# Kernel tuning notes

Measured on AMD Instinct MI355X. Metric: run time of the kernel, lower is better.

The kernel has to match this reference:

```python
import jax, jax.numpy as jnp
import numpy as np

NUM_CLASSES = 100000   # vocab (input_dim of the layer)
DIM = 256              # embedding dim (output_dim of the layer)
BATCH = 256
NUM_TRUE = 1024        # hardcoded num_true in call()
NUM_SAMPLED = 16384    # hardcoded num_sampled in call()
LOG_RANGE = float(np.log(NUM_CLASSES + 1.0))


def _sample_log_uniform_unique(rng, n, range_max):
    # Mimics tf log_uniform_candidate_sampler with unique=True: rejection-sample
    # from P(c) ~ log((c+2)/(c+1)) until n unique ids are collected.
    seen = {}
    log_range = np.log(range_max + 1.0)
    while len(seen) < n:
        u = rng.uniform(0.0, log_range, size=2 * n)
        ids = np.minimum(np.floor(np.exp(u) - 1.0).astype(np.int64), range_max - 1)
        for v in ids.tolist():
            if len(seen) >= n:
                break
            seen[v] = None
    return np.fromiter(seen.keys(), dtype=np.int64, count=n)


def setup_inputs() -> dict:
    key = jax.random.key(0)
    k1, k2, k3, k4 = jax.random.split(key, 4)
    inputs = jax.random.normal(k1, (BATCH, DIM), jnp.float32)
    # Original inits w/b to zeros; use small random values for a non-degenerate baseline.
    w = jax.random.normal(k2, (NUM_CLASSES, DIM), jnp.float32) * 0.02
    b = jax.random.normal(k3, (NUM_CLASSES,), jnp.float32) * 0.02
    labels = jax.random.randint(k4, (BATCH, NUM_TRUE), 0, NUM_CLASSES, dtype=jnp.int32)
    rng = np.random.default_rng(0)
    sampled = jnp.asarray(_sample_log_uniform_unique(rng, NUM_SAMPLED, NUM_CLASSES), jnp.int32)
    return {"inputs": inputs, "w": w, "b": b, "labels": labels, "sampled": sampled}


def _log_uniform_prob(ids):
    idf = ids.astype(jnp.float32)
    return jnp.log((idf + 2.0) / (idf + 1.0)) / LOG_RANGE


def _expected_count(ids):
    # P(id appears among NUM_SAMPLED unique candidates) = 1 - (1-p)^NUM_SAMPLED
    p = _log_uniform_prob(ids)
    return -jnp.expm1(NUM_SAMPLED * jnp.log1p(-p))


def _sigmoid_xent(logits, target):
    # numerically stable sigmoid cross-entropy, target is a scalar label value
    return jnp.maximum(logits, 0.0) - logits * target + jnp.log1p(jnp.exp(-jnp.abs(logits)))


def reference(inputs, w, b, labels, sampled):
    # true logits: per-example dot with each true class row  [B, T]
    true_w = w[labels]                                    # [B, T, D] gather
    true_logits = jnp.einsum('bd,btd->bt', inputs, true_w) + b[labels]
    true_logits = true_logits - jnp.log(_expected_count(labels))
    # sampled logits: shared candidate set  [B, S]
    sampled_logits = inputs @ w[sampled].T + b[sampled]
    sampled_logits = sampled_logits - jnp.log(_expected_count(sampled))
    # NCE targets: 1/num_true for true classes, 0 for sampled; sum over columns
    true_xent = _sigmoid_xent(true_logits, 1.0 / NUM_TRUE)
    sampled_xent = _sigmoid_xent(sampled_logits, 0.0)
    return true_xent.sum(axis=1) + sampled_xent.sum(axis=1)   # [B]
```

## Files before the change

kernel.cpp:

```cpp
#include <hip/hip_runtime.h>
#include <hip/hip_bf16.h>

#define NUM_CLASSES 100000
#define DIM 256
#define BATCH 256
#define NUM_TRUE 1024
#define NUM_SAMPLED 16384
#define LOG_RANGE 11.51293546492023f
#define INV_LOG_RANGE (1.0f / LOG_RANGE)

#define SBLOCKS 512
#define NBUCKET 3125
#define CAP     512
#define COMB_THREADS 100096

typedef __bf16 bf16x8 __attribute__((ext_vector_type(8)));
typedef float  f32x4  __attribute__((ext_vector_type(4)));

static __device__ __forceinline__ unsigned short f2bf(float f) {
    unsigned int u = __float_as_uint(f);
    unsigned int lsb = (u >> 16) & 1u;
    u += 0x7fffu + lsb;
    return (unsigned short)(u >> 16);
}

static __device__ __forceinline__ float neg_log_ec(int id) {
    float idf = (float)id;
    float p = logf((idf + 2.0f) / (idf + 1.0f)) * INV_LOG_RANGE;
    float ec = -expm1f((float)NUM_SAMPLED * log1pf(-p));
    return -logf(ec);
}

static __device__ __forceinline__ float dot4(float4 a, float4 b) {
    return fmaf(a.x, b.x, fmaf(a.y, b.y, fmaf(a.z, b.z, a.w * b.w)));
}

__global__ __launch_bounds__(256) void comb_kernel(const float* __restrict__ bias,
                                                   const float* __restrict__ inputs,
                                                   const int* __restrict__ labels,
                                                   float* __restrict__ comb,
                                                   unsigned short* __restrict__ inbf,
                                                   int* __restrict__ cursor,
                                                   unsigned int* __restrict__ pairs) {
    int c = blockIdx.x * 256 + threadIdx.x;
    if (c < NUM_CLASSES) comb[c] = bias[c] + neg_log_ec(c);
    if (c < BATCH * DIM) inbf[c] = f2bf(inputs[c]);
    for (int g = c; g < BATCH * NUM_TRUE; g += COMB_THREADS) {
        int lbl = labels[g];
        int bk = lbl >> 5;
        int pos = atomicAdd(&cursor[bk], 1);
        if (pos < CAP)
            pairs[(size_t)bk * CAP + pos] = ((unsigned int)(g >> 10) << 17) | (unsigned int)lbl;
    }
}

union SMem {
    struct { unsigned short lw[32][264]; float cs[32]; } s;
    struct { float rows[32][260]; float cmb[32]; } t;
};

__global__ __launch_bounds__(256) void fused_kernel(const float* __restrict__ inputs,
                                                    const float* __restrict__ w,
                                                    const float* __restrict__ comb,
                                                    const int* __restrict__ sampled,
                                                    const unsigned short* __restrict__ inbf,
                                                    const int* __restrict__ cursor,
                                                    const unsigned int* __restrict__ pairs,
                                                    float* __restrict__ ptrue,
                                                    float* __restrict__ partial) {
    __shared__ SMem u;
    __shared__ float bacc[BATCH];

    const int tid = threadIdx.x;

    if (blockIdx.x < SBLOCKS) {
        const int sblk = blockIdx.x;
        const int s0 = sblk * 32;
        bacc[tid] = 0.0f;

        const int inner = tid & 15;
        const int r16   = tid >> 4;
        #pragma unroll
        for (int rb = 0; rb < 2; ++rb) {
            const int r = rb * 16 + r16;
            const int id = sampled[s0 + r];
            const float* src = w + (size_t)id * DIM;
            #pragma unroll
            for (int j = 0; j < 4; ++j) {
                float4 v = *(const float4*)(src + j * 64 + inner * 4);
                ushort4 pk;
                pk.x = f2bf(v.x); pk.y = f2bf(v.y); pk.z = f2bf(v.z); pk.w = f2bf(v.w);
                *(ushort4*)(&u.s.lw[r][j * 64 + inner * 4]) = pk;
            }
        }
        if (tid < 32) u.s.cs[tid] = comb[sampled[s0 + tid]];
        __syncthreads();

        const int lane = tid & 63;
        const int wv   = tid >> 6;
        const int m    = lane & 15;
        const int quad = lane >> 4;
        const int shalf = (wv >> 1) * 16;
        const int bhalf = (wv & 1) * 128;

        bf16x8 af[8];
        #pragma unroll
        for (int kk = 0; kk < 8; ++kk)
            af[kk] = *(const bf16x8*)(&u.s.lw[shalf + m][kk * 32 + quad * 8]);

        #pragma unroll
        for (int t = 0; t < 8; ++t) {
            const int brow = bhalf + t * 16 + m;
            const unsigned short* bp = inbf + brow * DIM;
            bf16x8 bf[8];
            #pragma unroll
            for (int kk = 0; kk < 8; ++kk)
                bf[kk] = *(const bf16x8*)(bp + kk * 32 + quad * 8);
            f32x4 acc = {0, 0, 0, 0};
            #pragma unroll
            for (int kk = 0; kk < 8; ++kk)
                acc = __builtin_amdgcn_mfma_f32_16x16x32_bf16(af[kk], bf[kk], acc, 0, 0, 0);
            float ps = 0.0f;
            #pragma unroll
            for (int r = 0; r < 4; ++r) {
                float c = u.s.cs[shalf + quad * 4 + r];
                float l = acc[r] + c;
                ps += fmaxf(l, 0.0f) + __logf(1.0f + __expf(-fabsf(l)));
            }
            ps += __shfl_xor(ps, 16); ps += __shfl_xor(ps, 32);
            if (quad == 0) atomicAdd(&bacc[bhalf + t * 16 + m], ps);
        }
        __syncthreads();
        partial[tid * SBLOCKS + sblk] = bacc[tid];
    } else {
        const int tb = blockIdx.x - SBLOCKS;
        int n = cursor[tb];
        n = (n < CAP) ? n : CAP;
        bacc[tid] = 0.0f;

        if (n > 0) {
            const float* wb = w + (size_t)tb * (32 * DIM);
            #pragma unroll
            for (int j = 0; j < 8; ++j) {
                const int e = (tid + j * 256) * 4;
                float4 v = *(const float4*)(wb + e);
                *(float4*)&u.t.rows[e >> 8][e & 255] = v;
            }
            if (tid < 32) u.t.cmb[tid] = comb[tb * 32 + tid];
        }
        __syncthreads();

        if (n > 0) {
            const int gidx = tid >> 4;
            const int part = tid & 15;
            const float4* inp4 = (const float4*)inputs;
            const unsigned int* pb = pairs + (size_t)tb * CAP;
            for (int p = gidx; p < n; p += 16) {
                const unsigned int pk = pb[p];
                const int b = pk >> 17;
                const int r = pk & 31;
                float4 i0 = inp4[b * 64 + part];
                float4 i1 = inp4[b * 64 + 16 + part];
                float4 i2 = inp4[b * 64 + 32 + part];
                float4 i3 = inp4[b * 64 + 48 + part];
                float4 w0 = *(const float4*)&u.t.rows[r][part * 4];
                float4 w1 = *(const float4*)&u.t.rows[r][64 + part * 4];
                float4 w2 = *(const float4*)&u.t.rows[r][128 + part * 4];
                float4 w3 = *(const float4*)&u.t.rows[r][192 + part * 4];
                float d = dot4(w0, i0) + dot4(w1, i1) + dot4(w2, i2) + dot4(w3, i3);
                d += __shfl_xor(d, 1); d += __shfl_xor(d, 2);
                d += __shfl_xor(d, 4); d += __shfl_xor(d, 8);
                const float logit = d + u.t.cmb[r];
                const float v = fmaxf(logit, 0.0f) - logit * (1.0f / (float)NUM_TRUE)
                              + __logf(1.0f + __expf(-fabsf(logit)));
                if (part == 0) atomicAdd(&bacc[b], v);
            }
        }
        __syncthreads();
        ptrue[tb * 256 + tid] = bacc[tid];
    }
}

__global__ __launch_bounds__(256) void reduce_kernel(const float* __restrict__ partial,
                                                     const float* __restrict__ ptrue,
                                                     float* __restrict__ out) {
    __shared__ float wsum[4];
    const int b = blockIdx.x;
    const int tid = threadIdx.x;
    float v = partial[b * SBLOCKS + tid] + partial[b * SBLOCKS + 256 + tid];
    #pragma unroll
    for (int i = 0; i < 13; ++i) {
        const int k = tid * 13 + i;
        if (k < NBUCKET) v += ptrue[k * 256 + b];
    }
    v += __shfl_xor(v, 1);  v += __shfl_xor(v, 2);  v += __shfl_xor(v, 4);
    v += __shfl_xor(v, 8);  v += __shfl_xor(v, 16); v += __shfl_xor(v, 32);
    if ((tid & 63) == 0) wsum[tid >> 6] = v;
    __syncthreads();
    if (tid == 0) out[b] = wsum[0] + wsum[1] + wsum[2] + wsum[3];
}

extern "C" void kernel_launch(void* const* d_in, const int* in_sizes, int n_in,
                              void* d_out, int out_size, void* d_ws, size_t ws_size,
                              hipStream_t stream) {
    const float* inputs  = (const float*)d_in[0];
    const float* w       = (const float*)d_in[1];
    const float* bias    = (const float*)d_in[2];
    const int*   labels  = (const int*)d_in[3];
    const int*   sampled = (const int*)d_in[4];
    float* out = (float*)d_out;

    float*          comb    = (float*)d_ws;
    unsigned short* inbf    = (unsigned short*)((char*)d_ws + 409600);
    float*          partial = (float*)((char*)d_ws + 540672);
    float*          ptrue   = (float*)((char*)d_ws + 1064960);
    int*            cursor  = (int*)((char*)d_ws + 4264960);
    unsigned int*   pairs   = (unsigned int*)((char*)d_ws + 4280320);

    hipMemsetAsync(cursor, 0, NBUCKET * sizeof(int), stream);
    comb_kernel<<<(NUM_CLASSES + 255) / 256, 256, 0, stream>>>(bias, inputs, labels,
                                                               comb, inbf, cursor, pairs);
    fused_kernel<<<SBLOCKS + NBUCKET, 256, 0, stream>>>(inputs, w, comb, sampled,
                                                        inbf, cursor, pairs, ptrue, partial);
    reduce_kernel<<<BATCH, 256, 0, stream>>>(partial, ptrue, out);
}
```

Before: 223.0 us.

## Compute true-class logits densely with bf16 MFMA per bucket instead of gathered dots

Each true-label bucket block now converts its 32 weight rows to bf16 and computes the full 32x256 logit tile against all batch rows with MFMA, storing it in shared memory. Each (batch, label) pair then just looks up its logit and applies the cross-entropy, replacing per-pair fp32 dot products that re-read the input rows. The ptrue layout is transposed so the reduce kernel reads it coalesced. This does far more arithmetic per bucket (dense versus sparse) and lowers true-logit precision to bf16, and it now runs even for buckets with no pairs.

After: 282.7 us. 1.27x slower.

```diff
diff --git a/kernel.cpp b/kernel.cpp
--- a/kernel.cpp
+++ b/kernel.cpp
@@ -11,6 +11,7 @@
 
 #define SBLOCKS 512
 #define NBUCKET 3125
+#define NB2     3328
 #define CAP     512
 #define COMB_THREADS 100096
 
@@ -29,10 +30,6 @@
     float p = logf((idf + 2.0f) / (idf + 1.0f)) * INV_LOG_RANGE;
     float ec = -expm1f((float)NUM_SAMPLED * log1pf(-p));
     return -logf(ec);
-}
-
-static __device__ __forceinline__ float dot4(float4 a, float4 b) {
-    return fmaf(a.x, b.x, fmaf(a.y, b.y, fmaf(a.z, b.z, a.w * b.w)));
 }
 
 __global__ __launch_bounds__(256) void comb_kernel(const float* __restrict__ bias,
@@ -55,8 +52,8 @@
 }
 
 union SMem {
-    struct { unsigned short lw[32][264]; float cs[32]; } s;
-    struct { float rows[32][260]; float cmb[32]; } t;
+    unsigned short lw[32][264];
+    float          lgt[32][257];
 };
 
 __global__ __launch_bounds__(256) void fused_kernel(const float* __restrict__ inputs,
@@ -69,17 +66,25 @@
                                                     float* __restrict__ ptrue,
                                                     float* __restrict__ partial) {
     __shared__ SMem u;
+    __shared__ float cs[32];
     __shared__ float bacc[BATCH];
 
-    const int tid = threadIdx.x;
+    const int tid   = threadIdx.x;
+    const int inner = tid & 15;
+    const int r16   = tid >> 4;
+    const int lane  = tid & 63;
+    const int wv    = tid >> 6;
+    const int m     = lane & 15;
+    const int quad  = lane >> 4;
+    const int shalf = (wv >> 1) * 16;
+    const int bhalf = (wv & 1) * 128;
+
+    bacc[tid] = 0.0f;
 
     if (blockIdx.x < SBLOCKS) {
         const int sblk = blockIdx.x;
         const int s0 = sblk * 32;
-        bacc[tid] = 0.0f;
-
-        const int inner = tid & 15;
-        const int r16   = tid >> 4;
+
         #pragma unroll
         for (int rb = 0; rb < 2; ++rb) {
             const int r = rb * 16 + r16;
@@ -90,23 +95,16 @@
                 float4 v = *(const float4*)(src + j * 64 + inner * 4);
                 ushort4 pk;
                 pk.x = f2bf(v.x); pk.y = f2bf(v.y); pk.z = f2bf(v.z); pk.w = f2bf(v.w);
-                *(ushort4*)(&u.s.lw[r][j * 64 + inner * 4]) = pk;
+                *(ushort4*)(&u.lw[r][j * 64 + inner * 4]) = pk;
             }
         }
-        if (tid < 32) u.s.cs[tid] = comb[sampled[s0 + tid]];
-        __syncthreads();
-
-        const int lane = tid & 63;
-        const int wv   = tid >> 6;
-        const int m    = lane & 15;
-        const int quad = lane >> 4;
-        const int shalf = (wv >> 1) * 16;
-        const int bhalf = (wv & 1) * 128;
+        if (tid < 32) cs[tid] = comb[sampled[s0 + tid]];
+        __syncthreads();
 
         bf16x8 af[8];
         #pragma unroll
         for (int kk = 0; kk < 8; ++kk)
-            af[kk] = *(const bf16x8*)(&u.s.lw[shalf + m][kk * 32 + quad * 8]);
+            af[kk] = *(const bf16x8*)(&u.lw[shalf + m][kk * 32 + quad * 8]);
 
         #pragma unroll
         for (int t = 0; t < 8; ++t) {
@@ -123,7 +121,7 @@
             float ps = 0.0f;
             #pragma unroll
             for (int r = 0; r < 4; ++r) {
-                float c = u.s.cs[shalf + quad * 4 + r];
+                float c = cs[shalf + quad * 4 + r];
                 float l = acc[r] + c;
                 ps += fmaxf(l, 0.0f) + __logf(1.0f + __expf(-fabsf(l)));
             }
@@ -134,50 +132,62 @@
         partial[tid * SBLOCKS + sblk] = bacc[tid];
     } else {
         const int tb = blockIdx.x - SBLOCKS;
+        const int s0 = tb * 32;
+
+        const float* wb = w + (size_t)s0 * DIM;
+        #pragma unroll
+        for (int rb = 0; rb < 2; ++rb) {
+            const int r = rb * 16 + r16;
+            const float* src = wb + r * DIM;
+            #pragma unroll
+            for (int j = 0; j < 4; ++j) {
+                float4 v = *(const float4*)(src + j * 64 + inner * 4);
+                ushort4 pk;
+                pk.x = f2bf(v.x); pk.y = f2bf(v.y); pk.z = f2bf(v.z); pk.w = f2bf(v.w);
+                *(ushort4*)(&u.lw[r][j * 64 + inner * 4]) = pk;
+            }
+        }
+        if (tid < 32) cs[tid] = comb[s0 + tid];
+        __syncthreads();
+
+        bf16x8 af[8];
+        #pragma unroll
+        for (int kk = 0; kk < 8; ++kk)
+            af[kk] = *(const bf16x8*)(&u.lw[shalf + m][kk * 32 + quad * 8]);
+        __syncthreads();
+
+        #pragma unroll
+        for (int t = 0; t < 8; ++t) {
+            const int brow = bhalf + t * 16 + m;
+            const unsigned short* bp = inbf + brow * DIM;
+            bf16x8 bf[8];
+            #pragma unroll
+            for (int kk = 0; kk < 8; ++kk)
+                bf[kk] = *(const bf16x8*)(bp + kk * 32 + quad * 8);
+            f32x4 acc = {0, 0, 0, 0};
+            #pragma unroll
+            for (int kk = 0; kk < 8; ++kk)
+                acc = __builtin_amdgcn_mfma_f32_16x16x32_bf16(af[kk], bf[kk], acc, 0, 0, 0);
+            #pragma unroll
+            for (int r = 0; r < 4; ++r)
+                u.lgt[shalf + quad * 4 + r][brow] = acc[r] + cs[shalf + quad * 4 + r];
+        }
+        __syncthreads();
+
         int n = cursor[tb];
         n = (n < CAP) ? n : CAP;
-        bacc[tid] = 0.0f;
-
-        if (n > 0) {
-            const float* wb = w + (size_t)tb * (32 * DIM);
-            #pragma unroll
-            for (int j = 0; j < 8; ++j) {
-                const int e = (tid + j * 256) * 4;
-                float4 v = *(const float4*)(wb + e);
-                *(float4*)&u.t.rows[e >> 8][e & 255] = v;
-            }
-            if (tid < 32) u.t.cmb[tid] = comb[tb * 32 + tid];
-        }
-        __syncthreads();
-
-        if (n > 0) {
-            const int gidx = tid >> 4;
-            const int part = tid & 15;
-            const float4* inp4 = (const float4*)inputs;
-            const unsigned int* pb = pairs + (size_t)tb * CAP;
-            for (int p = gidx; p < n; p += 16) {
-                const unsigned int pk = pb[p];
-                const int b = pk >> 17;
-                const int r = pk & 31;
-                float4 i0 = inp4[b * 64 + part];
-                float4 i1 = inp4[b * 64 + 16 + part];
-                float4 i2 = inp4[b * 64 + 32 + part];
-                float4 i3 = inp4[b * 64 + 48 + part];
-                float4 w0 = *(const float4*)&u.t.rows[r][part * 4];
-                float4 w1 = *(const float4*)&u.t.rows[r][64 + part * 4];
-                float4 w2 = *(const float4*)&u.t.rows[r][128 + part * 4];
-                float4 w3 = *(const float4*)&u.t.rows[r][192 + part * 4];
-                float d = dot4(w0, i0) + dot4(w1, i1) + dot4(w2, i2) + dot4(w3, i3);
-                d += __shfl_xor(d, 1); d += __shfl_xor(d, 2);
-                d += __shfl_xor(d, 4); d += __shfl_xor(d, 8);
-                const float logit = d + u.t.cmb[r];
-                const float v = fmaxf(logit, 0.0f) - logit * (1.0f / (float)NUM_TRUE)
-                              + __logf(1.0f + __expf(-fabsf(logit)));
-                if (part == 0) atomicAdd(&bacc[b], v);
-            }
-        }
-        __syncthreads();
-        ptrue[tb * 256 + tid] = bacc[tid];
+        const unsigned int* pb = pairs + (size_t)tb * CAP;
+        for (int p = tid; p < n; p += 256) {
+            const unsigned int pk = pb[p];
+            const int b = pk >> 17;
+            const int r = pk & 31;
+            const float l = u.lgt[r][b];
+            const float v = fmaxf(l, 0.0f) - l * (1.0f / (float)NUM_TRUE)
+                          + __logf(1.0f + __expf(-fabsf(l)));
+            atomicAdd(&bacc[b], v);
+        }
+        __syncthreads();
+        ptrue[tid * NB2 + tb] = bacc[tid];
     }
 }
 
@@ -190,8 +200,8 @@
     float v = partial[b * SBLOCKS + tid] + partial[b * SBLOCKS + 256 + tid];
     #pragma unroll
     for (int i = 0; i < 13; ++i) {
-        const int k = tid * 13 + i;
-        if (k < NBUCKET) v += ptrue[k * 256 + b];
+        const int k = i * 256 + tid;
+        if (k < NBUCKET) v += ptrue[b * NB2 + k];
     }
     v += __shfl_xor(v, 1);  v += __shfl_xor(v, 2);  v += __shfl_xor(v, 4);
     v += __shfl_xor(v, 8);  v += __shfl_xor(v, 16); v += __shfl_xor(v, 32);
@@ -214,8 +224,8 @@
     unsigned short* inbf    = (unsigned short*)((char*)d_ws + 409600);
     float*          partial = (float*)((char*)d_ws + 540672);
     float*          ptrue   = (float*)((char*)d_ws + 1064960);
-    int*            cursor  = (int*)((char*)d_ws + 4264960);
-    unsigned int*   pairs   = (unsigned int*)((char*)d_ws + 4280320);
+    int*            cursor  = (int*)((char*)d_ws + 4472832);
+    unsigned int*   pairs   = (unsigned int*)((char*)d_ws + 4485632);
 
     hipMemsetAsync(cursor, 0, NBUCKET * sizeof(int), stream);
     comb_kernel<<<(NUM_CLASSES + 255) / 256, 256, 0, stream>>>(bias, inputs, labels,
```

## Compute full dense logits per class bucket with MFMA, mask sampled, reuse for true pairs

Applied to the files above, without the earlier changes.

Replaces the separate sampled-gather GEMM and scalar true-label dot products with a single dense bf16 MFMA pass over all vocabulary rows in 32-class buckets. Each block computes all 256x32 logits into shared memory, sums sigmoid-xent for classes flagged as sampled via a byte mask, and looks up true-pair logits from the same tile. This removes the scattered gather and the fp32 per-pair dot products, but computes logits for every class, about six times the sampled GEMM work, and true logits now use bf16 precision.

Result: slower. 239.0 us (+7.2%).

```diff
diff --git a/kernel.cpp b/kernel.cpp
--- a/kernel.cpp
+++ b/kernel.cpp
@@ -9,7 +9,6 @@
 #define LOG_RANGE 11.51293546492023f
 #define INV_LOG_RANGE (1.0f / LOG_RANGE)
 
-#define SBLOCKS 512
 #define NBUCKET 3125
 #define CAP     512
 #define COMB_THREADS 100096
@@ -31,20 +30,19 @@
     return -logf(ec);
 }
 
-static __device__ __forceinline__ float dot4(float4 a, float4 b) {
-    return fmaf(a.x, b.x, fmaf(a.y, b.y, fmaf(a.z, b.z, a.w * b.w)));
-}
-
 __global__ __launch_bounds__(256) void comb_kernel(const float* __restrict__ bias,
                                                    const float* __restrict__ inputs,
                                                    const int* __restrict__ labels,
+                                                   const int* __restrict__ sampled,
                                                    float* __restrict__ comb,
                                                    unsigned short* __restrict__ inbf,
+                                                   unsigned char* __restrict__ sam,
                                                    int* __restrict__ cursor,
                                                    unsigned int* __restrict__ pairs) {
     int c = blockIdx.x * 256 + threadIdx.x;
     if (c < NUM_CLASSES) comb[c] = bias[c] + neg_log_ec(c);
     if (c < BATCH * DIM) inbf[c] = f2bf(inputs[c]);
+    if (c < NUM_SAMPLED) sam[sampled[c]] = 1;
     for (int g = c; g < BATCH * NUM_TRUE; g += COMB_THREADS) {
         int lbl = labels[g];
         int bk = lbl >> 5;
@@ -54,144 +52,118 @@
     }
 }
 
-union SMem {
-    struct { unsigned short lw[32][264]; float cs[32]; } s;
-    struct { float rows[32][260]; float cmb[32]; } t;
-};
-
-__global__ __launch_bounds__(256) void fused_kernel(const float* __restrict__ inputs,
-                                                    const float* __restrict__ w,
+__global__ __launch_bounds__(256) void fused_kernel(const float* __restrict__ w,
                                                     const float* __restrict__ comb,
-                                                    const int* __restrict__ sampled,
                                                     const unsigned short* __restrict__ inbf,
+                                                    const unsigned char* __restrict__ sam,
                                                     const int* __restrict__ cursor,
                                                     const unsigned int* __restrict__ pairs,
-                                                    float* __restrict__ ptrue,
-                                                    float* __restrict__ partial) {
-    __shared__ SMem u;
+                                                    float* __restrict__ ptrue) {
+    __shared__ unsigned short lw[32][264];
+    __shared__ float lgt[BATCH][33];
+    __shared__ float cs[32];
+    __shared__ int   sf[32];
     __shared__ float bacc[BATCH];
 
     const int tid = threadIdx.x;
+    const int tb  = blockIdx.x;
+    const int s0  = tb * 32;
 
-    if (blockIdx.x < SBLOCKS) {
-        const int sblk = blockIdx.x;
-        const int s0 = sblk * 32;
-        bacc[tid] = 0.0f;
+    int n = cursor[tb];
+    n = (n < CAP) ? n : CAP;
 
-        const int inner = tid & 15;
-        const int r16   = tid >> 4;
+    bacc[tid] = 0.0f;
+
+    const int inner = tid & 15;
+    const int r16   = tid >> 4;
+    const float* wb = w + (size_t)s0 * DIM;
+    #pragma unroll
+    for (int rb = 0; rb < 2; ++rb) {
+        const int r = rb * 16 + r16;
+        const float* src = wb + r * DIM;
         #pragma unroll
-        for (int rb = 0; rb < 2; ++rb) {
-            const int r = rb * 16 + r16;
-            const int id = sampled[s0 + r];
-            const float* src = w + (size_t)id * DIM;
-            #pragma unroll
-            for (int j = 0; j < 4; ++j) {
-                float4 v = *(const float4*)(src + j * 64 + inner * 4);
-                ushort4 pk;
-                pk.x = f2bf(v.x); pk.y = f2bf(v.y); pk.z = f2bf(v.z); pk.w = f2bf(v.w);
-                *(ushort4*)(&u.s.lw[r][j * 64 + inner * 4]) = pk;
-            }
+        for (int j = 0; j < 4; ++j) {
+            float4 v = *(const float4*)(src + j * 64 + inner * 4);
+            ushort4 pk;
+            pk.x = f2bf(v.x); pk.y = f2bf(v.y); pk.z = f2bf(v.z); pk.w = f2bf(v.w);
+            *(ushort4*)(&lw[r][j * 64 + inner * 4]) = pk;
         }
-        if (tid < 32) u.s.cs[tid] = comb[sampled[s0 + tid]];
-        __syncthreads();
+    }
+    if (tid < 32) {
+        cs[tid] = comb[s0 + tid];
+        sf[tid] = (int)sam[s0 + tid];
+    }
+    __syncthreads();
 
-        const int lane = tid & 63;
-        const int wv   = tid >> 6;
-        const int m    = lane & 15;
-        const int quad = lane >> 4;
-        const int shalf = (wv >> 1) * 16;
-        const int bhalf = (wv & 1) * 128;
+    const int lane = tid & 63;
+    const int wv   = tid >> 6;
+    const int m    = lane & 15;
+    const int quad = lane >> 4;
+    const int rb0  = quad * 4;
 
-        bf16x8 af[8];
+    bf16x8 af0[8], af1[8];
+    #pragma unroll
+    for (int kk = 0; kk < 8; ++kk) {
+        af0[kk] = *(const bf16x8*)(&lw[m][kk * 32 + quad * 8]);
+        af1[kk] = *(const bf16x8*)(&lw[16 + m][kk * 32 + quad * 8]);
+    }
+    float cs0[4], cs1[4];
+    #pragma unroll
+    for (int r = 0; r < 4; ++r) { cs0[r] = cs[rb0 + r]; cs1[r] = cs[16 + rb0 + r]; }
+
+    #pragma unroll
+    for (int t = 0; t < 4; ++t) {
+        const int brow = wv * 64 + t * 16 + m;
+        const unsigned short* bp = inbf + brow * DIM;
+        bf16x8 bf[8];
         #pragma unroll
         for (int kk = 0; kk < 8; ++kk)
-            af[kk] = *(const bf16x8*)(&u.s.lw[shalf + m][kk * 32 + quad * 8]);
+            bf[kk] = *(const bf16x8*)(bp + kk * 32 + quad * 8);
+        f32x4 a0 = {0, 0, 0, 0}, a1 = {0, 0, 0, 0};
+        #pragma unroll
+        for (int kk = 0; kk < 8; ++kk) {
+            a0 = __builtin_amdgcn_mfma_f32_16x16x32_bf16(af0[kk], bf[kk], a0, 0, 0, 0);
+            a1 = __builtin_amdgcn_mfma_f32_16x16x32_bf16(af1[kk], bf[kk], a1, 0, 0, 0);
+        }
+        #pragma unroll
+        for (int r = 0; r < 4; ++r) {
+            lgt[brow][rb0 + r]      = a0[r] + cs0[r];
+            lgt[brow][16 + rb0 + r] = a1[r] + cs1[r];
+        }
+    }
+    __syncthreads();
 
-        #pragma unroll
-        for (int t = 0; t < 8; ++t) {
-            const int brow = bhalf + t * 16 + m;
-            const unsigned short* bp = inbf + brow * DIM;
-            bf16x8 bf[8];
-            #pragma unroll
-            for (int kk = 0; kk < 8; ++kk)
-                bf[kk] = *(const bf16x8*)(bp + kk * 32 + quad * 8);
-            f32x4 acc = {0, 0, 0, 0};
-            #pragma unroll
-            for (int kk = 0; kk < 8; ++kk)
-                acc = __builtin_amdgcn_mfma_f32_16x16x32_bf16(af[kk], bf[kk], acc, 0, 0, 0);
-            float ps = 0.0f;
-            #pragma unroll
-            for (int r = 0; r < 4; ++r) {
-                float c = u.s.cs[shalf + quad * 4 + r];
-                float l = acc[r] + c;
-                ps += fmaxf(l, 0.0f) + __logf(1.0f + __expf(-fabsf(l)));
-            }
-            ps += __shfl_xor(ps, 16); ps += __shfl_xor(ps, 32);
-            if (quad == 0) atomicAdd(&bacc[bhalf + t * 16 + m], ps);
+    float ps = 0.0f;
+    for (int r = 0; r < 32; ++r) {
+        if (sf[r]) {
+            const float l = lgt[tid][r];
+            ps += fmaxf(l, 0.0f) + __logf(1.0f + __expf(-fabsf(l)));
         }
-        __syncthreads();
-        partial[tid * SBLOCKS + sblk] = bacc[tid];
-    } else {
-        const int tb = blockIdx.x - SBLOCKS;
-        int n = cursor[tb];
-        n = (n < CAP) ? n : CAP;
-        bacc[tid] = 0.0f;
-
-        if (n > 0) {
-            const float* wb = w + (size_t)tb * (32 * DIM);
-            #pragma unroll
-            for (int j = 0; j < 8; ++j) {
-                const int e = (tid + j * 256) * 4;
-                float4 v = *(const float4*)(wb + e);
-                *(float4*)&u.t.rows[e >> 8][e & 255] = v;
-            }
-            if (tid < 32) u.t.cmb[tid] = comb[tb * 32 + tid];
-        }
-        __syncthreads();
-
-        if (n > 0) {
-            const int gidx = tid >> 4;
-            const int part = tid & 15;
-            const float4* inp4 = (const float4*)inputs;
-            const unsigned int* pb = pairs + (size_t)tb * CAP;
-            for (int p = gidx; p < n; p += 16) {
-                const unsigned int pk = pb[p];
-                const int b = pk >> 17;
-                const int r = pk & 31;
-                float4 i0 = inp4[b * 64 + part];
-                float4 i1 = inp4[b * 64 + 16 + part];
-                float4 i2 = inp4[b * 64 + 32 + part];
-                float4 i3 = inp4[b * 64 + 48 + part];
-                float4 w0 = *(const float4*)&u.t.rows[r][part * 4];
-                float4 w1 = *(const float4*)&u.t.rows[r][64 + part * 4];
-                float4 w2 = *(const float4*)&u.t.rows[r][128 + part * 4];
-                float4 w3 = *(const float4*)&u.t.rows[r][192 + part * 4];
-                float d = dot4(w0, i0) + dot4(w1, i1) + dot4(w2, i2) + dot4(w3, i3);
-                d += __shfl_xor(d, 1); d += __shfl_xor(d, 2);
-                d += __shfl_xor(d, 4); d += __shfl_xor(d, 8);
-                const float logit = d + u.t.cmb[r];
-                const float v = fmaxf(logit, 0.0f) - logit * (1.0f / (float)NUM_TRUE)
-                              + __logf(1.0f + __expf(-fabsf(logit)));
-                if (part == 0) atomicAdd(&bacc[b], v);
-            }
-        }
-        __syncthreads();
-        ptrue[tb * 256 + tid] = bacc[tid];
     }
+    const unsigned int* pb = pairs + (size_t)tb * CAP;
+    for (int p = tid; p < n; p += 256) {
+        const unsigned int pk = pb[p];
+        const int b = pk >> 17;
+        const int r = pk & 31;
+        const float l = lgt[b][r];
+        const float v = fmaxf(l, 0.0f) - l * (1.0f / (float)NUM_TRUE)
+                      + __logf(1.0f + __expf(-fabsf(l)));
+        atomicAdd(&bacc[b], v);
+    }
+    __syncthreads();
+    ptrue[(size_t)tb * 256 + tid] = ps + bacc[tid];
 }
 
-__global__ __launch_bounds__(256) void reduce_kernel(const float* __restrict__ partial,
-                                                     const float* __restrict__ ptrue,
+__global__ __launch_bounds__(256) void reduce_kernel(const float* __restrict__ ptrue,
                                                      float* __restrict__ out) {
     __shared__ float wsum[4];
     const int b = blockIdx.x;
     const int tid = threadIdx.x;
-    float v = partial[b * SBLOCKS + tid] + partial[b * SBLOCKS + 256 + tid];
+    float v = 0.0f;
     #pragma unroll
     for (int i = 0; i < 13; ++i) {
-        const int k = tid * 13 + i;
-        if (k < NBUCKET) v += ptrue[k * 256 + b];
+        const int k = tid + i * 256;
+        if (k < NBUCKET) v += ptrue[(size_t)k * 256 + b];
     }
     v += __shfl_xor(v, 1);  v += __shfl_xor(v, 2);  v += __shfl_xor(v, 4);
     v += __shfl_xor(v, 8);  v += __shfl_xor(v, 16); v += __shfl_xor(v, 32);
@@ -210,17 +182,16 @@
     const int*   sampled = (const int*)d_in[4];
     float* out = (float*)d_out;
 
-    float*          comb    = (float*)d_ws;
-    unsigned short* inbf    = (unsigned short*)((char*)d_ws + 409600);
-    float*          partial = (float*)((char*)d_ws + 540672);
-    float*          ptrue   = (float*)((char*)d_ws + 1064960);
-    int*            cursor  = (int*)((char*)d_ws + 4264960);
-    unsigned int*   pairs   = (unsigned int*)((char*)d_ws + 4280320);
+    float*          comb   = (float*)d_ws;
+    unsigned short* inbf   = (unsigned short*)((char*)d_ws + 409600);
+    float*          ptrue  = (float*)((char*)d_ws + 540672);
+    int*            cursor = (int*)((char*)d_ws + 3740672);
+    unsigned char*  sam    = (unsigned char*)((char*)d_ws + 3753216);
+    unsigned int*   pairs  = (unsigned int*)((char*)d_ws + 3853216);
 
-    hipMemsetAsync(cursor, 0, NBUCKET * sizeof(int), stream);
-    comb_kernel<<<(NUM_CLASSES + 255) / 256, 256, 0, stream>>>(bias, inputs, labels,
-                                                               comb, inbf, cursor, pairs);
-    fused_kernel<<<SBLOCKS + NBUCKET, 256, 0, stream>>>(inputs, w, comb, sampled,
-                                                        inbf, cursor, pairs, ptrue, partial);
-    reduce_kernel<<<BATCH, 256, 0, stream>>>(partial, ptrue, out);
+    hipMemsetAsync((char*)d_ws + 3740672, 0, 12544 + 100000, stream);
+    comb_kernel<<<COMB_THREADS / 256, 256, 0, stream>>>(bias, inputs, labels, sampled,
+                                                        comb, inbf, sam, cursor, pairs);
+    fused_kernel<<<NBUCKET, 256, 0, stream>>>(w, comb, inbf, sam, cursor, pairs, ptrue);
+    reduce_kernel<<<BATCH, 256, 0, stream>>>(ptrue, out);
 }
```
